# Kernel tuning notes

Hardware: AMD Instinct MI355X
Metric: run time of the kernel (lower is better)

The kernel has to match this reference:

```python
import jax, jax.numpy as jnp
import numpy as np

D_MODEL = 1024
NUM_HEADS = 16
D_HEAD = D_MODEL // NUM_HEADS


def setup_inputs() -> dict:
    key = jax.random.key(0)
    ks = jax.random.split(key, 7)
    B, S = 2, 2048
    scale = 1.0 / np.sqrt(D_MODEL)
    return {
        "x": jax.random.normal(ks[0], (B, S, D_MODEL), dtype=jnp.float32),
        "attn_weights": jnp.zeros((1,), dtype=jnp.float32),  # unused in original forward
        "Wq": jax.random.normal(ks[1], (D_MODEL, D_MODEL), dtype=jnp.float32) * scale,
        "Wk": jax.random.normal(ks[2], (D_MODEL, D_MODEL), dtype=jnp.float32) * scale,
        "Wv": jax.random.normal(ks[3], (D_MODEL, D_MODEL), dtype=jnp.float32) * scale,
        "Wp": jax.random.normal(ks[4], (D_MODEL, D_MODEL), dtype=jnp.float32) * scale,
        "bp": jnp.zeros((D_MODEL,), dtype=jnp.float32),
    }


def reference(x, attn_weights, Wq, Wk, Wv, Wp, bp):
    B, S, D = x.shape
    H, Dh = NUM_HEADS, D_HEAD
    # torch Linear: y = x @ W.T  (weights stored [out, in])
    q = (x @ Wq.T).reshape(B, S, H, Dh).transpose(0, 2, 1, 3)  # [B,H,S,Dh]
    k = (x @ Wk.T).reshape(B, S, H, Dh).transpose(0, 2, 1, 3)
    v = (x @ Wv.T).reshape(B, S, H, Dh).transpose(0, 2, 1, 3)
    # NOTE: original module applies NO 1/sqrt(d) scaling
    scores = jnp.einsum("bhqd,bhkd->bhqk", q, k)
    weights = jax.nn.softmax(scores, axis=-1)  # dropout is inference no-op
    out = jnp.einsum("bhqk,bhkd->bhqd", weights, v)
    out = out.transpose(0, 2, 1, 3).reshape(B, S, D)
    return out @ Wp.T + bp
```

## Files before the change

### kernel.cpp

```cpp
#include <hip/hip_runtime.h>
#include <hip/hip_bf16.h>

#define D_MODEL 1024
#define NUM_HEADS 16
#define D_HEAD 64
#define BATCH 2
#define SEQ 2048
#define TOKENS (BATCH * SEQ)

typedef __attribute__((ext_vector_type(8))) short bf16x8;
typedef __attribute__((ext_vector_type(4))) float f32x4;

typedef __attribute__((address_space(1))) const unsigned int as1_uint;
typedef __attribute__((address_space(3))) unsigned int as3_uint;

#define LOG2E 1.44269504088896340736f

static __device__ __forceinline__ unsigned short f2bf(float f) {
    unsigned int u = __builtin_bit_cast(unsigned int, f);
    u += 0x7fffu + ((u >> 16) & 1u);
    return (unsigned short)(u >> 16);
}

static __device__ __forceinline__ unsigned int pk2bf(float a, float b) {
    __hip_bfloat162 h = __float22bfloat162_rn(float2{a, b});
    unsigned int u;
    __builtin_memcpy(&u, &h, 4);
    return u;
}

static __device__ __forceinline__ float fast_exp2(float x) {
    return __builtin_amdgcn_exp2f(x);
}

__global__ __launch_bounds__(256) void convert_bf16(
    const float* __restrict__ x,  const float* __restrict__ Wq,
    const float* __restrict__ Wk, const float* __restrict__ Wv,
    const float* __restrict__ Wp,
    unsigned short* __restrict__ xb,  unsigned short* __restrict__ Wqb,
    unsigned short* __restrict__ Wkb, unsigned short* __restrict__ Wvb,
    unsigned short* __restrict__ Wpb)
{
    int v = blockIdx.x * 256 + threadIdx.x;
    const float* s;
    unsigned short* d;
    int off;
    if (v < (1 << 20)) { s = x; d = xb; off = v; }
    else {
        int u = v - (1 << 20);
        int w = u >> 18;
        off = u & ((1 << 18) - 1);
        s = (w == 0) ? Wq : (w == 1) ? Wk : (w == 2) ? Wv : Wp;
        d = (w == 0) ? Wqb : (w == 1) ? Wkb : (w == 2) ? Wvb : Wpb;
    }
    float4 f = ((const float4*)s)[off];
    ushort4 o = { f2bf(f.x), f2bf(f.y), f2bf(f.z), f2bf(f.w) };
    ((ushort4*)d)[off] = o;
}

__global__ __launch_bounds__(256) void qkv_gemm(
    const unsigned short* __restrict__ xb,
    const unsigned short* __restrict__ Wqb, const unsigned short* __restrict__ Wkb,
    const unsigned short* __restrict__ Wvb,
    unsigned short* __restrict__ Q, unsigned short* __restrict__ Kb,
    unsigned short* __restrict__ Vt)
{
    const int m0 = blockIdx.x * 128;
    const int n0 = blockIdx.y * 128;
    const unsigned short* W = (blockIdx.z == 0) ? Wqb : (blockIdx.z == 1) ? Wkb : Wvb;

    __shared__ __attribute__((aligned(16))) unsigned short lA[128 * 32];
    __shared__ __attribute__((aligned(16))) unsigned short lB[128 * 32];

    const int t = threadIdx.x;
    const int wave = t >> 6, lane = t & 63;
    const int wm = (wave & 1) * 64, wn = (wave >> 1) * 64;
    const int l15 = lane & 15, quad = lane >> 4;

    f32x4 acc[4][4];
#pragma unroll
    for (int i = 0; i < 4; i++)
#pragma unroll
        for (int j = 0; j < 4; j++) acc[i][j] = (f32x4)0.f;

    for (int k0 = 0; k0 < D_MODEL; k0 += 32) {
        __syncthreads();
#pragma unroll
        for (int i = 0; i < 2; i++) {
            int fbase = wave * 64 + i * 256;
            int f = fbase + lane;
            int row = f >> 2, c = f & 3;
            __builtin_amdgcn_global_load_lds(
                (as1_uint*)&xb[(size_t)(m0 + row) * D_MODEL + k0 + c * 8],
                (as3_uint*)&lA[fbase * 8], 16, 0, 0);
            __builtin_amdgcn_global_load_lds(
                (as1_uint*)&W[(size_t)(n0 + row) * D_MODEL + k0 + c * 8],
                (as3_uint*)&lB[fbase * 8], 16, 0, 0);
        }
        __syncthreads();

        bf16x8 a[4], b[4];
#pragma unroll
        for (int mt = 0; mt < 4; mt++)
            a[mt] = *(const bf16x8*)&lA[(wm + mt * 16 + l15) * 32 + quad * 8];
#pragma unroll
        for (int nt = 0; nt < 4; nt++)
            b[nt] = *(const bf16x8*)&lB[(wn + nt * 16 + l15) * 32 + quad * 8];
#pragma unroll
        for (int mt = 0; mt < 4; mt++)
#pragma unroll
            for (int nt = 0; nt < 4; nt++)
                acc[mt][nt] = __builtin_amdgcn_mfma_f32_16x16x32_bf16(
                    a[mt], b[nt], acc[mt][nt], 0, 0, 0);
    }

    if (blockIdx.z == 2) {
        const int b = m0 >> 11;
        const int srow = (m0 & 2047) + wm + quad * 4;
#pragma unroll
        for (int mt = 0; mt < 4; mt++)
#pragma unroll
            for (int nt = 0; nt < 4; nt++) {
                int col = n0 + wn + nt * 16 + l15;
                int h = col >> 6, dh = col & 63;
                ushort4 pk = { f2bf(acc[mt][nt][0]), f2bf(acc[mt][nt][1]),
                               f2bf(acc[mt][nt][2]), f2bf(acc[mt][nt][3]) };
                *(ushort4*)&Vt[(size_t)((b * 16 + h) * 64 + dh) * SEQ + srow + mt * 16] = pk;
            }
    } else {
        unsigned short* Yo = (blockIdx.z == 0) ? Q : Kb;
        const float sc = (blockIdx.z == 0) ? LOG2E : 1.0f;
#pragma unroll
        for (int mt = 0; mt < 4; mt++)
#pragma unroll
            for (int nt = 0; nt < 4; nt++)
#pragma unroll
                for (int r = 0; r < 4; r++) {
                    int row = m0 + wm + mt * 16 + quad * 4 + r;
                    int col = n0 + wn + nt * 16 + l15;
                    Yo[(size_t)row * D_MODEL + col] = f2bf(acc[mt][nt][r] * sc);
                }
    }
}

__global__ __launch_bounds__(512, 4) void attn(
    const unsigned short* __restrict__ Q, const unsigned short* __restrict__ K,
    const unsigned short* __restrict__ Vt, unsigned short* __restrict__ O)
{
    const int q0 = blockIdx.x * 128;
    const int bh = blockIdx.y;
    const int b = bh >> 4, h = bh & 15;
    const size_t base = (size_t)b * SEQ * D_MODEL + (size_t)h * D_HEAD;
    const size_t baseV = (size_t)bh * D_HEAD * SEQ;

    __shared__ __attribute__((aligned(16))) char smem[65536];
    unsigned short* lK0 = (unsigned short*)&smem[0];
    unsigned short* lV0 = (unsigned short*)&smem[16384];
    unsigned short* lP0 = (unsigned short*)&smem[32768];

    const int t = threadIdx.x;
    const int wave = t >> 6, lane = t & 63;
    const int l15 = lane & 15, quad = lane >> 4;
    const int wq = wave & 3;
    const int sh = wave >> 2;
    const int qw = q0 + wq * 32;
    const int sbase = sh * (SEQ / 2);

    unsigned short* lK  = lK0 + sh * 4096;
    unsigned short* lVt = lV0 + sh * 4096;
    unsigned short* lP  = lP0 + wave * 2048;

    bf16x8 bq[2][2];
#pragma unroll
    for (int mq = 0; mq < 2; mq++)
#pragma unroll
        for (int kk = 0; kk < 2; kk++)
            bq[mq][kk] = *(const bf16x8*)&Q[base +
                (size_t)(qw + mq * 16 + l15) * D_MODEL + kk * 32 + quad * 8];

    const int tl = t & 255;
    const int r0 = tl >> 3, c0 = tl & 7;
    const int cs = (c0 ^ (r0 & 7)) * 8;
    const unsigned short* gK0 = &K[base + (size_t)(sbase + r0) * D_MODEL + c0 * 8];
    const unsigned short* gK1 = &K[base + (size_t)(sbase + r0 + 32) * D_MODEL + c0 * 8];
    const unsigned short* gV0 = &Vt[baseV + (size_t)r0 * SEQ + sbase + c0 * 8];
    const unsigned short* gV1 = &Vt[baseV + (size_t)(r0 + 32) * SEQ + sbase + c0 * 8];

    const int sw = l15 & 7;

    f32x4 o_acc[2][4];
#pragma unroll
    for (int i = 0; i < 2; i++)
#pragma unroll
        for (int j = 0; j < 4; j++) o_acc[i][j] = (f32x4)0.f;
    float l_run[2] = {0.f, 0.f};

    uint4 rK0 = *(const uint4*)gK0;
    uint4 rK1 = *(const uint4*)gK1;
    uint4 rV0 = *(const uint4*)gV0;
    uint4 rV1 = *(const uint4*)gV1;

    for (int s0 = 0; s0 < SEQ / 2; s0 += 64) {
        __syncthreads();
        *(uint4*)&lK[r0 * 64 + cs]        = rK0;
        *(uint4*)&lK[(r0 + 32) * 64 + cs] = rK1;
        *(uint4*)&lVt[r0 * 64 + cs]        = rV0;
        *(uint4*)&lVt[(r0 + 32) * 64 + cs] = rV1;
        __syncthreads();

        int sn = (s0 + 64 < SEQ / 2) ? s0 + 64 : 0;
        rK0 = *(const uint4*)(gK0 + (size_t)sn * D_MODEL);
        rK1 = *(const uint4*)(gK1 + (size_t)sn * D_MODEL);
        rV0 = *(const uint4*)(gV0 + sn);
        rV1 = *(const uint4*)(gV1 + sn);

        f32x4 st[4][2];
#pragma unroll
        for (int mt = 0; mt < 4; mt++)
#pragma unroll
            for (int mq = 0; mq < 2; mq++) st[mt][mq] = (f32x4)0.f;
#pragma unroll
        for (int kk = 0; kk < 2; kk++) {
            const int cc = ((kk * 4 + quad) ^ sw) * 8;
#pragma unroll
            for (int mt = 0; mt < 4; mt++) {
                bf16x8 ak = *(const bf16x8*)&lK[(mt * 16 + l15) * 64 + cc];
#pragma unroll
                for (int mq = 0; mq < 2; mq++)
                    st[mt][mq] = __builtin_amdgcn_mfma_f32_16x16x32_bf16(
                        ak, bq[mq][kk], st[mt][mq], 0, 0, 0);
            }
        }

#pragma unroll
        for (int mq = 0; mq < 2; mq++)
#pragma unroll
            for (int mt = 0; mt < 4; mt++)
#pragma unroll
                for (int r = 0; r < 4; r++) {
                    float e = fast_exp2(st[mt][mq][r]);
                    st[mt][mq][r] = e;
                    l_run[mq] += e;
                }

#pragma unroll
        for (int mq = 0; mq < 2; mq++)
#pragma unroll
            for (int mt = 0; mt < 4; mt++) {
                uint2 pk = { pk2bf(st[mt][mq][0], st[mt][mq][1]),
                             pk2bf(st[mt][mq][2], st[mt][mq][3]) };
                int g = (mt * 4 + quad) ^ (sw << 1);
                *(uint2*)&lP[mq * 1024 + l15 * 64 + g * 4] = pk;
            }

#pragma unroll
        for (int kk = 0; kk < 2; kk++) {
            const int cc = ((kk * 4 + quad) ^ sw) * 8;
            bf16x8 bv[4];
#pragma unroll
            for (int nt = 0; nt < 4; nt++)
                bv[nt] = *(const bf16x8*)&lVt[(nt * 16 + l15) * 64 + cc];
            const int gp = ((kk * 8 + quad * 2) ^ (sw << 1)) * 4;
#pragma unroll
            for (int mq = 0; mq < 2; mq++) {
                bf16x8 ap = *(const bf16x8*)&lP[mq * 1024 + l15 * 64 + gp];
#pragma unroll
                for (int nt = 0; nt < 4; nt++)
                    o_acc[mq][nt] = __builtin_amdgcn_mfma_f32_16x16x32_bf16(
                        ap, bv[nt], o_acc[mq][nt], 0, 0, 0);
            }
        }
    }

#pragma unroll
    for (int mq = 0; mq < 2; mq++) {
        l_run[mq] += __shfl_xor(l_run[mq], 16);
        l_run[mq] += __shfl_xor(l_run[mq], 32);
    }

    float* sO = (float*)&smem[0];
    float* sL = (float*)&smem[36864];
    __syncthreads();
    if (sh == 1) {
#pragma unroll
        for (int mq = 0; mq < 2; mq++) {
            sL[wq * 32 + mq * 16 + l15] = l_run[mq];
#pragma unroll
            for (int nt = 0; nt < 4; nt++)
#pragma unroll
                for (int r = 0; r < 4; r++)
                    sO[(wq * 32 + mq * 16 + quad * 4 + r) * 68 + nt * 16 + l15] =
                        o_acc[mq][nt][r];
        }
    }
    __syncthreads();
    if (sh == 0) {
#pragma unroll
        for (int mq = 0; mq < 2; mq++) {
            float ltot = l_run[mq] + sL[wq * 32 + mq * 16 + l15];
            float inv[4];
#pragma unroll
            for (int r = 0; r < 4; r++) inv[r] = 1.f / __shfl(ltot, quad * 4 + r);
#pragma unroll
            for (int nt = 0; nt < 4; nt++)
#pragma unroll
                for (int r = 0; r < 4; r++) {
                    int row = qw + mq * 16 + quad * 4 + r;
                    float v = o_acc[mq][nt][r] +
                              sO[(wq * 32 + mq * 16 + quad * 4 + r) * 68 + nt * 16 + l15];
                    O[base + (size_t)row * D_MODEL + nt * 16 + l15] = f2bf(v * inv[r]);
                }
        }
    }
}

__global__ __launch_bounds__(256) void proj_gemm(
    const unsigned short* __restrict__ A, const unsigned short* __restrict__ W,
    const float* __restrict__ bias, float* __restrict__ out)
{
    const int m0 = blockIdx.x * 128;
    const int n0 = blockIdx.y * 128;

    __shared__ __attribute__((aligned(16))) unsigned short lA[128 * 32];
    __shared__ __attribute__((aligned(16))) unsigned short lB[128 * 32];

    const int t = threadIdx.x;
    const int wave = t >> 6, lane = t & 63;
    const int wm = (wave & 1) * 64, wn = (wave >> 1) * 64;
    const int l15 = lane & 15, quad = lane >> 4;

    f32x4 acc[4][4];
#pragma unroll
    for (int i = 0; i < 4; i++)
#pragma unroll
        for (int j = 0; j < 4; j++) acc[i][j] = (f32x4)0.f;

    for (int k0 = 0; k0 < D_MODEL; k0 += 32) {
        __syncthreads();
#pragma unroll
        for (int i = 0; i < 2; i++) {
            int fbase = wave * 64 + i * 256;
            int f = fbase + lane;
            int row = f >> 2, c = f & 3;
            __builtin_amdgcn_global_load_lds(
                (as1_uint*)&A[(size_t)(m0 + row) * D_MODEL + k0 + c * 8],
                (as3_uint*)&lA[fbase * 8], 16, 0, 0);
            __builtin_amdgcn_global_load_lds(
                (as1_uint*)&W[(size_t)(n0 + row) * D_MODEL + k0 + c * 8],
                (as3_uint*)&lB[fbase * 8], 16, 0, 0);
        }
        __syncthreads();

        bf16x8 a[4], b[4];
#pragma unroll
        for (int mt = 0; mt < 4; mt++)
            a[mt] = *(const bf16x8*)&lA[(wm + mt * 16 + l15) * 32 + quad * 8];
#pragma unroll
        for (int nt = 0; nt < 4; nt++)
            b[nt] = *(const bf16x8*)&lB[(wn + nt * 16 + l15) * 32 + quad * 8];
#pragma unroll
        for (int mt = 0; mt < 4; mt++)
#pragma unroll
            for (int nt = 0; nt < 4; nt++)
                acc[mt][nt] = __builtin_amdgcn_mfma_f32_16x16x32_bf16(
                    a[mt], b[nt], acc[mt][nt], 0, 0, 0);
    }

#pragma unroll
    for (int mt = 0; mt < 4; mt++)
#pragma unroll
        for (int nt = 0; nt < 4; nt++)
#pragma unroll
            for (int r = 0; r < 4; r++) {
                int row = m0 + wm + mt * 16 + quad * 4 + r;
                int col = n0 + wn + nt * 16 + l15;
                out[(size_t)row * D_MODEL + col] = acc[mt][nt][r] + bias[col];
            }
}

extern "C" void kernel_launch(void* const* d_in, const int* in_sizes, int n_in,
                              void* d_out, int out_size, void* d_ws, size_t ws_size,
                              hipStream_t stream)
{
    const float* x  = (const float*)d_in[0];
    const float* Wq = (const float*)d_in[2];
    const float* Wk = (const float*)d_in[3];
    const float* Wv = (const float*)d_in[4];
    const float* Wp = (const float*)d_in[5];
    const float* bp = (const float*)d_in[6];
    float* out = (float*)d_out;

    unsigned short* Q   = (unsigned short*)d_ws;
    unsigned short* K   = Q   + (size_t)TOKENS * D_MODEL;
    unsigned short* Vt  = K   + (size_t)TOKENS * D_MODEL;
    unsigned short* O   = Vt  + (size_t)TOKENS * D_MODEL;
    unsigned short* xb  = O   + (size_t)TOKENS * D_MODEL;
    unsigned short* Wqb = xb  + (size_t)TOKENS * D_MODEL;
    unsigned short* Wkb = Wqb + (size_t)D_MODEL * D_MODEL;
    unsigned short* Wvb = Wkb + (size_t)D_MODEL * D_MODEL;
    unsigned short* Wpb = Wvb + (size_t)D_MODEL * D_MODEL;

    convert_bf16<<<8192, 256, 0, stream>>>(x, Wq, Wk, Wv, Wp,
                                           xb, Wqb, Wkb, Wvb, Wpb);
    qkv_gemm<<<dim3(TOKENS / 128, D_MODEL / 128, 3), 256, 0, stream>>>(
        xb, Wqb, Wkb, Wvb, Q, K, Vt);
    attn<<<dim3(SEQ / 128, BATCH * NUM_HEADS), 512, 0, stream>>>(Q, K, Vt, O);
    proj_gemm<<<dim3(TOKENS / 128, D_MODEL / 128), 256, 0, stream>>>(O, Wpb, bp, out);
}
```

Before: 207.0 us.

## Double GEMM K-tile with XOR-swizzled LDS and compute softmax row sums via MFMA

The QKV and projection GEMMs now stage 64-wide K slices per barrier pair instead of 32, halving the number of sync rounds. Columns are XOR-swizzled on the global-to-LDS load and the fragment reads use the matching swizzle to avoid bank conflicts. In attention, the per-row softmax denominator is accumulated by an extra MFMA of P against a ones vector, which replaces the scalar adds and the final shuffles. The costs are double the LDS per GEMM block, one extra MFMA per PV step, and row sums taken from bf16-rounded P rather than fp32.

```diff
diff --git a/kernel.cpp b/kernel.cpp
--- a/kernel.cpp
+++ b/kernel.cpp
@@ -69,13 +69,14 @@
     const int n0 = blockIdx.y * 128;
     const unsigned short* W = (blockIdx.z == 0) ? Wqb : (blockIdx.z == 1) ? Wkb : Wvb;
 
-    __shared__ __attribute__((aligned(16))) unsigned short lA[128 * 32];
-    __shared__ __attribute__((aligned(16))) unsigned short lB[128 * 32];
+    __shared__ __attribute__((aligned(16))) unsigned short lA[128 * 64];
+    __shared__ __attribute__((aligned(16))) unsigned short lB[128 * 64];
 
     const int t = threadIdx.x;
     const int wave = t >> 6, lane = t & 63;
     const int wm = (wave & 1) * 64, wn = (wave >> 1) * 64;
     const int l15 = lane & 15, quad = lane >> 4;
+    const int sw = l15 & 7;
 
     f32x4 acc[4][4];
 #pragma unroll
@@ -83,13 +84,14 @@
 #pragma unroll
         for (int j = 0; j < 4; j++) acc[i][j] = (f32x4)0.f;
 
-    for (int k0 = 0; k0 < D_MODEL; k0 += 32) {
-        __syncthreads();
-#pragma unroll
-        for (int i = 0; i < 2; i++) {
+    for (int k0 = 0; k0 < D_MODEL; k0 += 64) {
+        __syncthreads();
+#pragma unroll
+        for (int i = 0; i < 4; i++) {
             int fbase = wave * 64 + i * 256;
             int f = fbase + lane;
-            int row = f >> 2, c = f & 3;
+            int row = f >> 3, cp = f & 7;
+            int c = cp ^ (row & 7);
             __builtin_amdgcn_global_load_lds(
                 (as1_uint*)&xb[(size_t)(m0 + row) * D_MODEL + k0 + c * 8],
                 (as3_uint*)&lA[fbase * 8], 16, 0, 0);
@@ -99,19 +101,23 @@
         }
         __syncthreads();
 
-        bf16x8 a[4], b[4];
-#pragma unroll
-        for (int mt = 0; mt < 4; mt++)
-            a[mt] = *(const bf16x8*)&lA[(wm + mt * 16 + l15) * 32 + quad * 8];
-#pragma unroll
-        for (int nt = 0; nt < 4; nt++)
-            b[nt] = *(const bf16x8*)&lB[(wn + nt * 16 + l15) * 32 + quad * 8];
-#pragma unroll
-        for (int mt = 0; mt < 4; mt++)
-#pragma unroll
-            for (int nt = 0; nt < 4; nt++)
-                acc[mt][nt] = __builtin_amdgcn_mfma_f32_16x16x32_bf16(
-                    a[mt], b[nt], acc[mt][nt], 0, 0, 0);
+#pragma unroll
+        for (int kk = 0; kk < 2; kk++) {
+            const int cc = ((kk * 4 + quad) ^ sw) * 8;
+            bf16x8 a[4], b[4];
+#pragma unroll
+            for (int mt = 0; mt < 4; mt++)
+                a[mt] = *(const bf16x8*)&lA[(wm + mt * 16 + l15) * 64 + cc];
+#pragma unroll
+            for (int nt = 0; nt < 4; nt++)
+                b[nt] = *(const bf16x8*)&lB[(wn + nt * 16 + l15) * 64 + cc];
+#pragma unroll
+            for (int mt = 0; mt < 4; mt++)
+#pragma unroll
+                for (int nt = 0; nt < 4; nt++)
+                    acc[mt][nt] = __builtin_amdgcn_mfma_f32_16x16x32_bf16(
+                        a[mt], b[nt], acc[mt][nt], 0, 0, 0);
+        }
     }
 
     if (blockIdx.z == 2) {
@@ -170,6 +176,10 @@
     unsigned short* lVt = lV0 + sh * 4096;
     unsigned short* lP  = lP0 + wave * 2048;
 
+    bf16x8 ones;
+#pragma unroll
+    for (int i = 0; i < 8; i++) ones[i] = (short)0x3F80;
+
     bf16x8 bq[2][2];
 #pragma unroll
     for (int mq = 0; mq < 2; mq++)
@@ -193,7 +203,9 @@
     for (int i = 0; i < 2; i++)
 #pragma unroll
         for (int j = 0; j < 4; j++) o_acc[i][j] = (f32x4)0.f;
-    float l_run[2] = {0.f, 0.f};
+    f32x4 o_l[2];
+#pragma unroll
+    for (int i = 0; i < 2; i++) o_l[i] = (f32x4)0.f;
 
     uint4 rK0 = *(const uint4*)gK0;
     uint4 rK1 = *(const uint4*)gK1;
@@ -237,11 +249,8 @@
 #pragma unroll
             for (int mt = 0; mt < 4; mt++)
 #pragma unroll
-                for (int r = 0; r < 4; r++) {
-                    float e = fast_exp2(st[mt][mq][r]);
-                    st[mt][mq][r] = e;
-                    l_run[mq] += e;
-                }
+                for (int r = 0; r < 4; r++)
+                    st[mt][mq][r] = fast_exp2(st[mt][mq][r]);
 
 #pragma unroll
         for (int mq = 0; mq < 2; mq++)
@@ -268,14 +277,10 @@
                 for (int nt = 0; nt < 4; nt++)
                     o_acc[mq][nt] = __builtin_amdgcn_mfma_f32_16x16x32_bf16(
                         ap, bv[nt], o_acc[mq][nt], 0, 0, 0);
+                o_l[mq] = __builtin_amdgcn_mfma_f32_16x16x32_bf16(
+                    ap, ones, o_l[mq], 0, 0, 0);
             }
         }
-    }
-
-#pragma unroll
-    for (int mq = 0; mq < 2; mq++) {
-        l_run[mq] += __shfl_xor(l_run[mq], 16);
-        l_run[mq] += __shfl_xor(l_run[mq], 32);
     }
 
     float* sO = (float*)&smem[0];
@@ -284,7 +289,9 @@
     if (sh == 1) {
 #pragma unroll
         for (int mq = 0; mq < 2; mq++) {
-            sL[wq * 32 + mq * 16 + l15] = l_run[mq];
+#pragma unroll
+            for (int r = 0; r < 4; r++)
+                sL[wq * 32 + mq * 16 + quad * 4 + r] = o_l[mq][r];
 #pragma unroll
             for (int nt = 0; nt < 4; nt++)
 #pragma unroll
@@ -297,10 +304,10 @@
     if (sh == 0) {
 #pragma unroll
         for (int mq = 0; mq < 2; mq++) {
-            float ltot = l_run[mq] + sL[wq * 32 + mq * 16 + l15];
             float inv[4];
 #pragma unroll
-            for (int r = 0; r < 4; r++) inv[r] = 1.f / __shfl(ltot, quad * 4 + r);
+            for (int r = 0; r < 4; r++)
+                inv[r] = 1.f / (o_l[mq][r] + sL[wq * 32 + mq * 16 + quad * 4 + r]);
 #pragma unroll
             for (int nt = 0; nt < 4; nt++)
 #pragma unroll
@@ -321,13 +328,14 @@
     const int m0 = blockIdx.x * 128;
     const int n0 = blockIdx.y * 128;
 
-    __shared__ __attribute__((aligned(16))) unsigned short lA[128 * 32];
-    __shared__ __attribute__((aligned(16))) unsigned short lB[128 * 32];
+    __shared__ __attribute__((aligned(16))) unsigned short lA[128 * 64];
+    __shared__ __attribute__((aligned(16))) unsigned short lB[128 * 64];
 
     const int t = threadIdx.x;
     const int wave = t >> 6, lane = t & 63;
     const int wm = (wave & 1) * 64, wn = (wave >> 1) * 64;
     const int l15 = lane & 15, quad = lane >> 4;
+    const int sw = l15 & 7;
 
     f32x4 acc[4][4];
 #pragma unroll
@@ -335,13 +343,14 @@
 #pragma unroll
         for (int j = 0; j < 4; j++) acc[i][j] = (f32x4)0.f;
 
-    for (int k0 = 0; k0 < D_MODEL; k0 += 32) {
-        __syncthreads();
-#pragma unroll
-        for (int i = 0; i < 2; i++) {
+    for (int k0 = 0; k0 < D_MODEL; k0 += 64) {
+        __syncthreads();
+#pragma unroll
+        for (int i = 0; i < 4; i++) {
             int fbase = wave * 64 + i * 256;
             int f = fbase + lane;
-            int row = f >> 2, c = f & 3;
+            int row = f >> 3, cp = f & 7;
+            int c = cp ^ (row & 7);
             __builtin_amdgcn_global_load_lds(
                 (as1_uint*)&A[(size_t)(m0 + row) * D_MODEL + k0 + c * 8],
                 (as3_uint*)&lA[fbase * 8], 16, 0, 0);
@@ -351,19 +360,23 @@
         }
         __syncthreads();
 
-        bf16x8 a[4], b[4];
-#pragma unroll
-        for (int mt = 0; mt < 4; mt++)
-            a[mt] = *(const bf16x8*)&lA[(wm + mt * 16 + l15) * 32 + quad * 8];
-#pragma unroll
-        for (int nt = 0; nt < 4; nt++)
-            b[nt] = *(const bf16x8*)&lB[(wn + nt * 16 + l15) * 32 + quad * 8];
-#pragma unroll
-        for (int mt = 0; mt < 4; mt++)
-#pragma unroll
-            for (int nt = 0; nt < 4; nt++)
-                acc[mt][nt] = __builtin_amdgcn_mfma_f32_16x16x32_bf16(
-                    a[mt], b[nt], acc[mt][nt], 0, 0, 0);
+#pragma unroll
+        for (int kk = 0; kk < 2; kk++) {
+            const int cc = ((kk * 4 + quad) ^ sw) * 8;
+            bf16x8 a[4], b[4];
+#pragma unroll
+            for (int mt = 0; mt < 4; mt++)
+                a[mt] = *(const bf16x8*)&lA[(wm + mt * 16 + l15) * 64 + cc];
+#pragma unroll
+            for (int nt = 0; nt < 4; nt++)
+                b[nt] = *(const bf16x8*)&lB[(wn + nt * 16 + l15) * 64 + cc];
+#pragma unroll
+            for (int mt = 0; mt < 4; mt++)
+#pragma unroll
+                for (int nt = 0; nt < 4; nt++)
+                    acc[mt][nt] = __builtin_amdgcn_mfma_f32_16x16x32_bf16(
+                        a[mt], b[nt], acc[mt][nt], 0, 0, 0);
+        }
     }
 
 #pragma unroll
```

Result: faster. 198.3 us, median of 2 (-4.2%).
